# Kernel optimization log

Hardware: AMD Instinct MI355X
Metric: run time of the kernel (lower is better)

The kernel has to match this reference:

```python
import jax, jax.numpy as jnp
import numpy as np


def setup_inputs() -> dict:
    key = jax.random.key(0)
    k1, k2, k3 = jax.random.split(key, 3)
    N, D, E = 4096, 1024, 8  # tokens, d_model, path_num (experts)
    x = jax.random.normal(k1, (N, D), dtype=jnp.float32)
    score = jax.random.uniform(k2, (N, E), dtype=jnp.float32)
    hot_mask = jax.random.randint(k3, (N, E), 0, 2).astype(jnp.int32)
    tag = jnp.arange(N, dtype=jnp.int32).reshape(N, 1)
    return {"x": x, "score": score, "hot_mask": hot_mask, "tag": tag}


def reference(x, score, hot_mask, tag):
    # Per-expert gather dispatch with score scaling (route_logic='1d', transform=True).
    # Torch version produces variable-length per-expert flows; here each expert's
    # output is packed into a fixed capacity of N slots (selected tokens first,
    # in original order, matching torch.nonzero ordering), zero-padded beyond count.
    N, D = x.shape
    E = hot_mask.shape[1]
    mask = hot_mask > 0  # [N, E] multi-hot routing mask
    pos = jnp.arange(N)

    def dispatch(mask_e, score_e):
        # stable partition: selected tokens get their index, others index+N
        order = jnp.argsort(jnp.where(mask_e, pos, pos + N))  # [N]
        count = mask_e.sum()
        valid = pos < count  # [N] first `count` slots hold real tokens
        data = x * score_e[:, None]  # transform: scale by routing score
        out_data = jnp.where(valid[:, None], data[order], 0.0)  # [N, D]
        out_tag = jnp.where(valid[:, None], tag[order], 0)      # [N, 1]
        return out_data, out_tag, count

    out_data, out_tags, counts = jax.vmap(dispatch, in_axes=(1, 1))(mask, score)
    # out_data: [E, N, D], out_tags: [E, N, 1], counts: [E]
    return out_data, out_tags, counts
```

## Files before the change

kernel.cpp:

```cpp
#include <hip/hip_runtime.h>

#define N_TOK 4096
#define DMODEL 1024
#define NEXP 8
#define RPB 16

typedef float vfloat4 __attribute__((ext_vector_type(4)));

__global__ __launch_bounds__(1024) void dispatch_fused(
        const float* __restrict__ x,
        const float* __restrict__ score,
        const int*   __restrict__ hot_mask,
        float* __restrict__ out_data,
        float* __restrict__ out_tags,
        float* __restrict__ out_cnts)
{
    const int row0  = blockIdx.x * RPB;
    const int e     = row0 >> 12;
    const int slot0 = row0 & (N_TOK - 1);
    const int tid   = threadIdx.x;
    const int wave  = tid >> 6;
    const int lane  = tid & 63;

    __shared__ int   wsum[64];
    __shared__ int   s_n[RPB];
    __shared__ float s_sc[RPB];

    if (tid < RPB) s_n[tid] = -1;

    unsigned long long bal[4];
#pragma unroll
    for (int j = 0; j < 4; ++j) {
        const int tok = j * 1024 + tid;
        const int m = (hot_mask[(size_t)tok * NEXP + e] > 0) ? 1 : 0;
        bal[j] = __ballot(m);
        if (lane == 0) wsum[j * 16 + wave] = (int)__popcll(bal[j]);
    }
    __syncthreads();

    if (wave == 0) {
        int v = wsum[lane];
#pragma unroll
        for (int off = 1; off < 64; off <<= 1) {
            int u = __shfl_up(v, off);
            if (lane >= off) v += u;
        }
        wsum[lane] = v;
    }
    __syncthreads();

#pragma unroll
    for (int j = 0; j < 4; ++j) {
        if ((bal[j] >> lane) & 1ull) {
            const int idx = j * 16 + wave;
            const int slot = (idx ? wsum[idx - 1] : 0)
                           + (int)__popcll(bal[j] & ((1ull << lane) - 1ull));
            const int r = slot - slot0;
            if (0 <= r && r < RPB) s_n[r] = j * 1024 + tid;
        }
    }
    __syncthreads();

    if (tid < RPB) {
        const int n = s_n[tid];
        out_tags[row0 + tid] = (n >= 0) ? (float)n : 0.0f;
        s_sc[tid] = (n >= 0) ? score[(size_t)n * NEXP + e] : 0.0f;
    }
    if (slot0 == 0 && tid == 0) out_cnts[e] = (float)wsum[63];
    __syncthreads();

    const int t  = tid & 255;
    const int r0 = tid >> 8;
#pragma unroll
    for (int i = 0; i < 4; ++i) {
        const int r = r0 + 4 * i;
        const int n = s_n[r];
        vfloat4* orow = reinterpret_cast<vfloat4*>(
            out_data + (size_t)(row0 + r) * DMODEL) + t;
        vfloat4 v;
        if (n >= 0) {
            v = reinterpret_cast<const vfloat4*>(x + (size_t)n * DMODEL)[t];
            v *= s_sc[r];
        } else {
            v = (vfloat4)(0.f);
        }
        __builtin_nontemporal_store(v, orow);
    }
}

extern "C" void kernel_launch(void* const* d_in, const int* in_sizes, int n_in,
                              void* d_out, int out_size, void* d_ws, size_t ws_size,
                              hipStream_t stream) {
    const float* x        = (const float*)d_in[0];
    const float* score    = (const float*)d_in[1];
    const int*   hot_mask = (const int*)d_in[2];

    float* out      = (float*)d_out;
    float* out_data = out;
    float* out_tags = out + (size_t)NEXP * N_TOK * DMODEL;
    float* out_cnts = out_tags + (size_t)NEXP * N_TOK;

    dispatch_fused<<<(NEXP * N_TOK) / RPB, 1024, 0, stream>>>(
        x, score, hot_mask, out_data, out_tags, out_cnts);
}
```

Measured before the change: 37.65 us.

## Scatter from input-token chunks and zero-fill tail in separate ranges

Each block now owns a 64-token input chunk per expert rather than 16 output slots. It computes its output slots from a full-column prefix scan and scatters the scaled selected rows to those slots, while the zero tail is split evenly across the chunks. The grid shrinks from 2048 blocks of 1024 threads to 512 blocks of 256 threads, so the redundant per-block mask scan runs far fewer times. In exchange each block does more serial row work, stores are no longer nontemporal, and per-block load depends on how many tokens are selected.

```diff
diff --git a/kernel.cpp b/kernel.cpp
--- a/kernel.cpp
+++ b/kernel.cpp
@@ -3,11 +3,11 @@
 #define N_TOK 4096
 #define DMODEL 1024
 #define NEXP 8
-#define RPB 16
+#define NCHUNK 64
 
 typedef float vfloat4 __attribute__((ext_vector_type(4)));
 
-__global__ __launch_bounds__(1024) void dispatch_fused(
+__global__ __launch_bounds__(256) void dispatch_one(
         const float* __restrict__ x,
         const float* __restrict__ score,
         const int*   __restrict__ hot_mask,
@@ -15,26 +15,26 @@
         float* __restrict__ out_tags,
         float* __restrict__ out_cnts)
 {
-    const int row0  = blockIdx.x * RPB;
-    const int e     = row0 >> 12;
-    const int slot0 = row0 & (N_TOK - 1);
-    const int tid   = threadIdx.x;
-    const int wave  = tid >> 6;
-    const int lane  = tid & 63;
+    const int b    = blockIdx.x;
+    const int e    = b >> 6;
+    const int c    = b & (NCHUNK - 1);
+    const int tid  = threadIdx.x;
+    const int wave = tid >> 6;
+    const int lane = tid & 63;
 
-    __shared__ int   wsum[64];
-    __shared__ int   s_n[RPB];
-    __shared__ float s_sc[RPB];
+    __shared__ int   wsum[NCHUNK];
+    __shared__ int   scan[NCHUNK];
+    __shared__ int   s_tok[64];
+    __shared__ int   s_slot[64];
+    __shared__ float s_sc[64];
+    __shared__ int   s_nsel;
 
-    if (tid < RPB) s_n[tid] = -1;
-
-    unsigned long long bal[4];
 #pragma unroll
-    for (int j = 0; j < 4; ++j) {
-        const int tok = j * 1024 + tid;
+    for (int j = 0; j < 16; ++j) {
+        const int tok = j * 256 + tid;
         const int m = (hot_mask[(size_t)tok * NEXP + e] > 0) ? 1 : 0;
-        bal[j] = __ballot(m);
-        if (lane == 0) wsum[j * 16 + wave] = (int)__popcll(bal[j]);
+        const unsigned long long bal = __ballot(m);
+        if (lane == 0) wsum[j * 4 + wave] = (int)__popcll(bal);
     }
     __syncthreads();
 
@@ -45,47 +45,47 @@
             int u = __shfl_up(v, off);
             if (lane >= off) v += u;
         }
-        wsum[lane] = v;
+        scan[lane] = v;
     }
     __syncthreads();
+    const int cnt  = scan[NCHUNK - 1];
+    const int pref = c ? scan[c - 1] : 0;
 
-#pragma unroll
-    for (int j = 0; j < 4; ++j) {
-        if ((bal[j] >> lane) & 1ull) {
-            const int idx = j * 16 + wave;
-            const int slot = (idx ? wsum[idx - 1] : 0)
-                           + (int)__popcll(bal[j] & ((1ull << lane) - 1ull));
-            const int r = slot - slot0;
-            if (0 <= r && r < RPB) s_n[r] = j * 1024 + tid;
+    if (wave == 0) {
+        const int tok = c * 64 + lane;
+        const int m = (hot_mask[(size_t)tok * NEXP + e] > 0) ? 1 : 0;
+        const unsigned long long bal = __ballot(m);
+        if (lane == 0) s_nsel = (int)__popcll(bal);
+        if (m) {
+            const int idx = (int)__popcll(bal & ((1ull << lane) - 1ull));
+            const int sl = pref + idx;
+            s_tok[idx]  = tok;
+            s_slot[idx] = sl;
+            s_sc[idx]   = score[(size_t)tok * NEXP + e];
+            out_tags[e * N_TOK + sl] = (float)tok;
         }
     }
     __syncthreads();
+    const int nsel = s_nsel;
 
-    if (tid < RPB) {
-        const int n = s_n[tid];
-        out_tags[row0 + tid] = (n >= 0) ? (float)n : 0.0f;
-        s_sc[tid] = (n >= 0) ? score[(size_t)n * NEXP + e] : 0.0f;
+    for (int i = 0; i < nsel; ++i) {
+        const int tok = s_tok[i];
+        vfloat4 v = reinterpret_cast<const vfloat4*>(x + (size_t)tok * DMODEL)[tid];
+        v *= s_sc[i];
+        reinterpret_cast<vfloat4*>(
+            out_data + ((size_t)e * N_TOK + s_slot[i]) * DMODEL)[tid] = v;
     }
-    if (slot0 == 0 && tid == 0) out_cnts[e] = (float)wsum[63];
-    __syncthreads();
 
-    const int t  = tid & 255;
-    const int r0 = tid >> 8;
-#pragma unroll
-    for (int i = 0; i < 4; ++i) {
-        const int r = r0 + 4 * i;
-        const int n = s_n[r];
-        vfloat4* orow = reinterpret_cast<vfloat4*>(
-            out_data + (size_t)(row0 + r) * DMODEL) + t;
-        vfloat4 v;
-        if (n >= 0) {
-            v = reinterpret_cast<const vfloat4*>(x + (size_t)n * DMODEL)[t];
-            v *= s_sc[r];
-        } else {
-            v = (vfloat4)(0.f);
-        }
-        __builtin_nontemporal_store(v, orow);
-    }
+    const int sh = (N_TOK - cnt + NCHUNK - 1) >> 6;
+    const int lo = cnt + c * sh;
+    const int hi = min(lo + sh, N_TOK);
+    const vfloat4 z = (vfloat4)(0.f);
+    for (int r = lo; r < hi; ++r)
+        reinterpret_cast<vfloat4*>(
+            out_data + ((size_t)e * N_TOK + r) * DMODEL)[tid] = z;
+    if (lo + tid < hi) out_tags[e * N_TOK + lo + tid] = 0.0f;
+
+    if (c == 0 && tid == 0) out_cnts[e] = (float)cnt;
 }
 
 extern "C" void kernel_launch(void* const* d_in, const int* in_sizes, int n_in,
@@ -100,6 +100,6 @@
     float* out_tags = out + (size_t)NEXP * N_TOK * DMODEL;
     float* out_cnts = out_tags + (size_t)NEXP * N_TOK;
 
-    dispatch_fused<<<(NEXP * N_TOK) / RPB, 1024, 0, stream>>>(
+    dispatch_one<<<NEXP * NCHUNK, 256, 0, stream>>>(
         x, score, hot_mask, out_data, out_tags, out_cnts);
 }
```

Measured after the change: 32.64 us, median of 2. 13.3% less time.
